# Optimization experiments

Measured on AMD Instinct MI355X. Metric: run time of the kernel, lower is better.

The kernel has to match this reference:

```python
import jax, jax.numpy as jnp
import numpy as np

B, T, I, H = 64, 512, 1024, 1024


def setup_inputs() -> dict:
    key = jax.random.key(0)
    ks = jax.random.split(key, 6)
    s_ih = 1.0 / np.sqrt(I)
    s_hh = 1.0 / np.sqrt(H)
    x = jax.random.normal(ks[0], (B, T, I), dtype=jnp.float32)
    w_ih = jax.random.uniform(ks[1], (4 * H, I), minval=-s_ih, maxval=s_ih, dtype=jnp.float32)
    b_ih = jax.random.uniform(ks[2], (4 * H,), minval=-s_ih, maxval=s_ih, dtype=jnp.float32)
    w_hh = jax.random.uniform(ks[3], (4 * H, H), minval=-s_hh, maxval=s_hh, dtype=jnp.float32)
    b_hh = jax.random.uniform(ks[4], (4 * H,), minval=-s_hh, maxval=s_hh, dtype=jnp.float32)
    # forget_bias = logit(u), u ~ Uniform(1/H, 1-1/H), as in init_hidden
    u = jax.random.uniform(ks[5], (H,), minval=1.0 / H, maxval=1.0 - 1.0 / H, dtype=jnp.float32)
    forget_bias = jnp.log(u / (1.0 - u))
    h0 = jnp.zeros((B, H), dtype=jnp.float32)
    c0 = jnp.zeros((B, H), dtype=jnp.float32)
    return {"x": x, "w_ih": w_ih, "b_ih": b_ih, "w_hh": w_hh, "b_hh": b_hh,
            "forget_bias": forget_bias, "h0": h0, "c0": c0}


def reference(x, w_ih, b_ih, w_hh, b_hh, forget_bias, h0, c0):
    Hd = forget_bias.shape[0]
    # Precompute input projection for all timesteps: [T, B, 4H]
    xW = jnp.einsum('bti,gi->tbg', x, w_ih) + b_ih

    def step(carry, xw_t):
        h, c = carry
        lin = xw_t + h @ w_hh.T + b_hh  # [B, 4H]
        r, f, u, o = jnp.split(lin, 4, axis=1)
        r = jax.nn.sigmoid(r - forget_bias)
        f = jax.nn.sigmoid(f + forget_bias)
        u = jnp.tanh(u)
        o = jax.nn.sigmoid(o)
        g = r * (1.0 - (1.0 - f) ** 2) + (1.0 - r) * f ** 2  # UR gate
        c = g * c + (1.0 - g) * u
        h = o * jnp.tanh(c)
        return (h, c), h

    (h_t, c_t), out = jax.lax.scan(step, (h0, c0), xW)
    out = jnp.swapaxes(out, 0, 1)  # [B, T, H]
    return out, h_t[None], c_t[None]  # h/c with num_layers=1 leading dim
```

## Files before the change

kernel.cpp:

```cpp
#include <hip/hip_runtime.h>
#include <stdint.h>
#include <stddef.h>

typedef __attribute__((ext_vector_type(8))) short short8;
typedef __attribute__((ext_vector_type(4))) float f32x4;
typedef __attribute__((ext_vector_type(2))) float f32x2;

#define MFMA16(A, B, C) __builtin_amdgcn_mfma_f32_16x16x32_bf16((A), (B), (C), 0, 0, 0)

static const size_t OFF_WIH  = 67108864;
static const size_t OFF_WHH  = 75497472;
static const size_t OFF_BIAS = 83886080;
static const size_t OFF_H0   = 83902464;
static const size_t OFF_H1   = 84033536;
static const size_t OFF_FLG  = 84164608;
static const size_t OFF_XW   = 84426752;
static const size_t XW_F32_BYTES = 536870912;

__device__ __forceinline__ unsigned short f2bf(float f) {
    union { float f; uint32_t u; } v; v.f = f;
    uint32_t u = v.u;
    u += 0x7FFFu + ((u >> 16) & 1u);
    return (unsigned short)(u >> 16);
}
__device__ __forceinline__ float bf2f(unsigned short b) {
    union { uint32_t u; float f; } v; v.u = ((uint32_t)b) << 16;
    return v.f;
}

__device__ __forceinline__ float fast_sigmoid(float x) {
    return 1.f / (1.f + __expf(-x));
}
__device__ __forceinline__ float fast_tanh(float x) {
    return 1.f - 2.f / (__expf(2.f * x) + 1.f);
}

__global__ __launch_bounds__(256) void cast4_kernel(const float* __restrict__ s,
                                                    unsigned short* __restrict__ d, int n4) {
    int i = blockIdx.x * 256 + threadIdx.x;
    if (i >= n4) return;
    float4 f = ((const float4*)s)[i];
    ushort4 o;
    o.x = f2bf(f.x); o.y = f2bf(f.y); o.z = f2bf(f.z); o.w = f2bf(f.w);
    ((ushort4*)d)[i] = o;
}

__global__ __launch_bounds__(256) void init_misc(const float* __restrict__ b_ih,
                                                 const float* __restrict__ b_hh,
                                                 float* __restrict__ bias,
                                                 const float* __restrict__ h0,
                                                 unsigned short* __restrict__ h_ini,
                                                 unsigned int* __restrict__ flags) {
    int i = blockIdx.x * 256 + threadIdx.x;
    if (i < 512) flags[i] = 0u;
    if (i < 4096) bias[i] = b_ih[i] + b_hh[i];
    if (i < 65536) h_ini[i] = f2bf(h0[i]);
}

template <bool XWF32>
__global__ __launch_bounds__(512, 2) void fused_kernel(
        unsigned short* hb0, unsigned short* hb1,
        void* xw,
        const unsigned short* __restrict__ whh,
        const unsigned short* __restrict__ wih,
        const float* __restrict__ x,
        const float* __restrict__ bias,
        const float* __restrict__ fb,
        const float* __restrict__ c0,
        float* __restrict__ out,
        float* __restrict__ hcout,
        unsigned int* flags) {
    __shared__ __align__(16) char smem[131072];
    const int tid = threadIdx.x;
    const int wave = tid >> 6, lane = tid & 63;
    unsigned int* xwprog = flags + 256;

    if (blockIdx.x >= 64) {
        unsigned short* As = (unsigned short*)smem;
        unsigned short* Bs = (unsigned short*)(smem + 8192);
        const int g = blockIdx.x - 64;
        const int wm = (wave & 3) * 32, wn = (wave >> 2) * 64;
        const int lr = lane & 15, lk = (lane >> 4) * 8;
        const int r0 = tid >> 2, k0c = (tid & 3) * 8;
        const int rbase = (lane >> 4) * 4;

        for (int tau = g; tau < 8192; tau += 192) {
            const int bm = tau >> 5, bn = tau & 31;
            const int m = bm * 128 + r0;
            const float* pax = x + (size_t)((m & 63) * 512 + (m >> 6)) * 1024 + k0c;
            const unsigned short* pbw = wih + (size_t)(bn * 128 + r0) * 1024 + k0c;
            unsigned short* sa = As + r0 * 32 + k0c;
            unsigned short* sb = Bs + r0 * 32 + k0c;

            f32x4 acc[2][4] = {};
            for (int kk = 0; kk < 32; ++kk) {
                const int ko = kk * 32;
                float4 a0 = *(const float4*)(pax + ko);
                float4 a1 = *(const float4*)(pax + ko + 4);
                uint4 bv = *(const uint4*)(pbw + ko);
                __syncthreads();
                ushort4 ca, cb;
                ca.x = f2bf(a0.x); ca.y = f2bf(a0.y); ca.z = f2bf(a0.z); ca.w = f2bf(a0.w);
                cb.x = f2bf(a1.x); cb.y = f2bf(a1.y); cb.z = f2bf(a1.z); cb.w = f2bf(a1.w);
                *(ushort4*)sa = ca;
                *(ushort4*)(sa + 4) = cb;
                *(uint4*)sb = bv;
                __syncthreads();
                short8 af0 = *(const short8*)(As + (wm + lr) * 32 + lk);
                short8 af1 = *(const short8*)(As + (wm + 16 + lr) * 32 + lk);
                short8 bf4[4];
#pragma unroll
                for (int ni = 0; ni < 4; ++ni)
                    bf4[ni] = *(const short8*)(Bs + (wn + ni * 16 + lr) * 32 + lk);
#pragma unroll
                for (int ni = 0; ni < 4; ++ni) {
                    acc[0][ni] = MFMA16(af0, bf4[ni], acc[0][ni]);
                    acc[1][ni] = MFMA16(af1, bf4[ni], acc[1][ni]);
                }
            }
#pragma unroll
            for (int ni = 0; ni < 4; ++ni) {
                const int gc = bn * 128 + wn + ni * 16 + lr;
                const float bvs = bias[gc];
#pragma unroll
                for (int mi = 0; mi < 2; ++mi) {
                    const int gr = bm * 128 + wm + mi * 16 + rbase;
#pragma unroll
                    for (int r = 0; r < 4; ++r) {
                        const float v = acc[mi][ni][r] + bvs;
                        if constexpr (XWF32) {
                            float* p = (float*)xw + (size_t)(gr + r) * 4096 + gc;
                            asm volatile("global_store_dword %0, %1, off sc1"
                                         :: "v"(p), "v"(v) : "memory");
                        } else {
                            unsigned short* p = (unsigned short*)xw + (size_t)(gr + r) * 4096 + gc;
                            const unsigned int hv = f2bf(v);
                            asm volatile("global_store_short %0, %1, off sc1"
                                         :: "v"(p), "v"(hv) : "memory");
                        }
                    }
                }
            }
            asm volatile("s_waitcnt vmcnt(0)" ::: "memory");
            __syncthreads();
            if (tid == 0)
                __hip_atomic_fetch_add(&xwprog[bm], 1u, __ATOMIC_RELAXED,
                                       __HIP_MEMORY_SCOPE_AGENT);
        }
        return;
    }

    float* part = (float*)smem;
    const int bk = blockIdx.x, ch0 = bk * 16;
    const int kq = wave;
    const int lr = lane & 15, g = lane >> 4;
    unsigned int* ctr = flags;

    short8 Wf[4][4];
#pragma unroll
    for (int ni = 0; ni < 4; ++ni)
#pragma unroll
        for (int ks = 0; ks < 4; ++ks) {
            const unsigned short* p = whh + (size_t)(ni * 1024 + ch0 + lr) * 1024
                                          + kq * 128 + ks * 32 + g * 8;
            asm volatile("global_load_dwordx4 %0, %1, off"
                         : "=&v"(Wf[ni][ks]) : "v"(p));
        }
    asm volatile("s_waitcnt vmcnt(0)" ::: "memory");
    __builtin_amdgcn_sched_barrier(0);

    const int b  = tid >> 3;
    const int j0 = 2 * (tid & 7);
    const int ch = ch0 + j0;
    const float fb0 = fb[ch], fb1 = fb[ch + 1];
    float c0r = c0[b * 1024 + ch], c1r = c0[b * 1024 + ch + 1];

    int wsl[4];
#pragma unroll
    for (int oi = 0; oi < 4; ++oi)
        wsl[oi] = kq * 4096 + lr * 64 + (((oi * 4 + g) ^ (lr & 7)) * 4);
    int rsl[4];
#pragma unroll
    for (int g4 = 0; g4 < 4; ++g4)
        rsl[g4] = b * 64 + (((g4 * 4 + (j0 >> 2)) ^ (b & 7)) * 4) + (j0 & 3);

    const float* xwf = (const float*)xw + (size_t)b * 4096 + ch;
    const unsigned short* xwb = (const unsigned short*)xw + (size_t)b * 4096 + ch;
    float* orun = out + (size_t)b * 524288 + ch;
    unsigned int* my_sig  = &ctr[(bk >> 3) * 32];
    unsigned int* my_poll = &ctr[kq * 32];

    {
        const unsigned int* pr0 = &xwprog[0];
        while (__hip_atomic_load(pr0, __ATOMIC_RELAXED, __HIP_MEMORY_SCOPE_AGENT) < 32u) {}
    }
    __builtin_amdgcn_sched_barrier(0);
    f32x2 xf[4];
    uint32_t xu[4];
    if constexpr (XWF32) {
        asm volatile(
            "global_load_dwordx2 %0, %4, off sc1\n\t"
            "global_load_dwordx2 %1, %5, off sc1\n\t"
            "global_load_dwordx2 %2, %6, off sc1\n\t"
            "global_load_dwordx2 %3, %7, off sc1"
            : "=&v"(xf[0]), "=&v"(xf[1]), "=&v"(xf[2]), "=&v"(xf[3])
            : "v"(xwf), "v"(xwf + 1024), "v"(xwf + 2048), "v"(xwf + 3072));
    } else {
        asm volatile(
            "global_load_dword %0, %4, off sc1\n\t"
            "global_load_dword %1, %5, off sc1\n\t"
            "global_load_dword %2, %6, off sc1\n\t"
            "global_load_dword %3, %7, off sc1"
            : "=&v"(xu[0]), "=&v"(xu[1]), "=&v"(xu[2]), "=&v"(xu[3])
            : "v"(xwb), "v"(xwb + 1024), "v"(xwb + 2048), "v"(xwb + 3072));
    }
    asm volatile("s_waitcnt vmcnt(0)" ::: "memory");
    __builtin_amdgcn_sched_barrier(0);

    float h0v = 0.f, h1v = 0.f;

    for (int t = 0; t < 512; ++t) {
        const unsigned short* hp = (t & 1) ? hb1 : hb0;
        unsigned short* hn       = (t & 1) ? hb0 : hb1;

        if (t > 0) {
            const unsigned tgt = (unsigned)t * 8u;
            while (__hip_atomic_load(my_poll, __ATOMIC_RELAXED,
                                     __HIP_MEMORY_SCOPE_AGENT) < tgt) {}
        }
        __builtin_amdgcn_sched_barrier(0);

        short8 af[4][4];
        {
            const unsigned short* hbase = hp + (size_t)lr * 1024 + kq * 128 + g * 8;
#pragma unroll
            for (int bi = 0; bi < 4; ++bi) {
                const unsigned short* p = hbase + (size_t)bi * 16 * 1024;
                asm volatile(
                    "global_load_dwordx4 %0, %4, off sc1\n\t"
                    "global_load_dwordx4 %1, %4, off offset:64 sc1\n\t"
                    "global_load_dwordx4 %2, %4, off offset:128 sc1\n\t"
                    "global_load_dwordx4 %3, %4, off offset:192 sc1"
                    : "=&v"(af[bi][0]), "=&v"(af[bi][1]),
                      "=&v"(af[bi][2]), "=&v"(af[bi][3])
                    : "v"(p));
            }
        }
        asm volatile("s_waitcnt vmcnt(0)" ::: "memory");
        __builtin_amdgcn_sched_barrier(0);

        f32x4 acc[4][4] = {};
#pragma unroll
        for (int ks = 0; ks < 4; ++ks)
#pragma unroll
            for (int oi = 0; oi < 4; ++oi)
#pragma unroll
                for (int bi = 0; bi < 4; ++bi)
                    acc[oi][bi] = MFMA16(Wf[oi][ks], af[bi][ks], acc[oi][bi]);

#pragma unroll
        for (int oi = 0; oi < 4; ++oi)
#pragma unroll
            for (int bi = 0; bi < 4; ++bi)
                *(f32x4*)&part[wsl[oi] + bi * 1024] = acc[oi][bi];
        __syncthreads();

        float l0[4], l1[4];
#pragma unroll
        for (int g4 = 0; g4 < 4; ++g4) {
            float s0, s1;
            if constexpr (XWF32) { s0 = xf[g4].x; s1 = xf[g4].y; }
            else { s0 = bf2f((unsigned short)xu[g4]);
                   s1 = bf2f((unsigned short)(xu[g4] >> 16)); }
#pragma unroll
            for (int k8 = 0; k8 < 8; ++k8) {
                const float2 v = *(const float2*)&part[k8 * 4096 + rsl[g4]];
                s0 += v.x; s1 += v.y;
            }
            l0[g4] = s0; l1[g4] = s1;
        }
        const float rg0 = fast_sigmoid(l0[0] - fb0);
        const float fg0 = fast_sigmoid(l0[1] + fb0);
        const float ug0 = fast_tanh(l0[2]);
        const float og0 = fast_sigmoid(l0[3]);
        const float rg1 = fast_sigmoid(l1[0] - fb1);
        const float fg1 = fast_sigmoid(l1[1] + fb1);
        const float ug1 = fast_tanh(l1[2]);
        const float og1 = fast_sigmoid(l1[3]);
        const float of0 = 1.f - fg0, of1 = 1.f - fg1;
        const float gg0 = rg0 * (1.f - of0 * of0) + (1.f - rg0) * (fg0 * fg0);
        const float gg1 = rg1 * (1.f - of1 * of1) + (1.f - rg1) * (fg1 * fg1);
        c0r = gg0 * c0r + (1.f - gg0) * ug0;
        c1r = gg1 * c1r + (1.f - gg1) * ug1;
        h0v = og0 * fast_tanh(c0r);
        h1v = og1 * fast_tanh(c1r);

        const unsigned hw = ((unsigned)f2bf(h1v) << 16) | (unsigned)f2bf(h0v);
        __hip_atomic_store((unsigned int*)&hn[b * 1024 + ch], hw,
                           __ATOMIC_RELAXED, __HIP_MEMORY_SCOPE_AGENT);

        __syncthreads();
        if (tid == 0)
            __hip_atomic_fetch_add(my_sig, 1u, __ATOMIC_RELAXED,
                                   __HIP_MEMORY_SCOPE_AGENT);
        __builtin_amdgcn_sched_barrier(0);

        *(f32x2*)orun = (f32x2){h0v, h1v};
        orun += 1024;
        {
            const int tp = (t < 511) ? t + 1 : 511;
            if (!(tp & 1)) {
                const unsigned int* pr = &xwprog[tp >> 1];
                while (__hip_atomic_load(pr, __ATOMIC_RELAXED,
                                         __HIP_MEMORY_SCOPE_AGENT) < 32u) {}
            }
            if constexpr (XWF32) {
                const float* p0 = xwf + (size_t)tp * 262144;
                asm volatile(
                    "global_load_dwordx2 %0, %4, off sc1\n\t"
                    "global_load_dwordx2 %1, %5, off sc1\n\t"
                    "global_load_dwordx2 %2, %6, off sc1\n\t"
                    "global_load_dwordx2 %3, %7, off sc1"
                    : "=&v"(xf[0]), "=&v"(xf[1]), "=&v"(xf[2]), "=&v"(xf[3])
                    : "v"(p0), "v"(p0 + 1024), "v"(p0 + 2048), "v"(p0 + 3072));
            } else {
                const unsigned short* p0 = xwb + (size_t)tp * 262144;
                asm volatile(
                    "global_load_dword %0, %4, off sc1\n\t"
                    "global_load_dword %1, %5, off sc1\n\t"
                    "global_load_dword %2, %6, off sc1\n\t"
                    "global_load_dword %3, %7, off sc1"
                    : "=&v"(xu[0]), "=&v"(xu[1]), "=&v"(xu[2]), "=&v"(xu[3])
                    : "v"(p0), "v"(p0 + 1024), "v"(p0 + 2048), "v"(p0 + 3072));
            }
        }
        asm volatile("s_waitcnt vmcnt(0)" ::: "memory");
        __builtin_amdgcn_sched_barrier(0);
    }

    *(f32x2*)&hcout[b * 1024 + ch] = (f32x2){h0v, h1v};
    *(f32x2*)&hcout[65536 + b * 1024 + ch] = (f32x2){c0r, c1r};
}

extern "C" void kernel_launch(void* const* d_in, const int* in_sizes, int n_in,
                              void* d_out, int out_size, void* d_ws, size_t ws_size,
                              hipStream_t stream) {
    const float* x   = (const float*)d_in[0];
    const float* wih = (const float*)d_in[1];
    const float* bih = (const float*)d_in[2];
    const float* whh = (const float*)d_in[3];
    const float* bhh = (const float*)d_in[4];
    const float* fb  = (const float*)d_in[5];
    const float* h0  = (const float*)d_in[6];
    const float* c0  = (const float*)d_in[7];

    char* ws = (char*)d_ws;
    float* out = (float*)d_out;
    float* hc  = out + 33554432;

    unsigned short* wihb = (unsigned short*)(ws + OFF_WIH);
    unsigned short* whhb = (unsigned short*)(ws + OFF_WHH);
    float* bias          = (float*)(ws + OFF_BIAS);
    unsigned short* hb0  = (unsigned short*)(ws + OFF_H0);
    unsigned short* hb1  = (unsigned short*)(ws + OFF_H1);
    unsigned int* flags  = (unsigned int*)(ws + OFF_FLG);
    void* xw             = (void*)(ws + OFF_XW);

    const bool f32path = ws_size >= OFF_XW + XW_F32_BYTES;

    cast4_kernel<<<4096, 256, 0, stream>>>(wih, wihb, 1048576);
    cast4_kernel<<<4096, 256, 0, stream>>>(whh, whhb, 1048576);
    init_misc<<<256, 256, 0, stream>>>(bih, bhh, bias, h0, hb0, flags);

    const float* xp = x;
    const float* fbp = fb;
    const float* c0p = c0;
    void* xwp = xw;
    const unsigned short* whhp = whhb;
    const unsigned short* wihp = wihb;
    const float* biasp = bias;
    void* kargs[] = { &hb0, &hb1, &xwp, &whhp, &wihp, &xp, &biasp, &fbp, &c0p,
                      &out, &hc, &flags };
    if (f32path)
        hipLaunchCooperativeKernel((void*)fused_kernel<true>, dim3(256), dim3(512),
                                   kargs, 0, stream);
    else
        hipLaunchCooperativeKernel((void*)fused_kernel<false>, dim3(256), dim3(512),
                                   kargs, 0, stream);
}
```

Baseline: 3.690 ms.

## Repartition recurrent LSTM steps to 128 full-K blocks without cross-wave reduction

The recurrent phase moves from 64 blocks, each splitting K across waves with a shared-memory partial-sum reduction, to 128 blocks that each own 8 channels. Every wave now holds the full K range of W_hh in registers, so the smem reduction and its syncs go away, and smaller shared memory may allow higher occupancy. Wave 0 polls eight group counters in parallel before a block barrier, h loads are double-buffered against the MFMAs, and xW producer polling now sleeps between checks. In exchange there are twice as many recurrent blocks to synchronize each step and fewer blocks left for the input projection. It also relies on the unseen launch code changing the grid to match.

```diff
diff --git a/kernel.cpp b/kernel.cpp
--- a/kernel.cpp
+++ b/kernel.cpp
@@ -4,7 +4,6 @@
 
 typedef __attribute__((ext_vector_type(8))) short short8;
 typedef __attribute__((ext_vector_type(4))) float f32x4;
-typedef __attribute__((ext_vector_type(2))) float f32x2;
 
 #define MFMA16(A, B, C) __builtin_amdgcn_mfma_f32_16x16x32_bf16((A), (B), (C), 0, 0, 0)
 
@@ -70,21 +69,21 @@
         float* __restrict__ out,
         float* __restrict__ hcout,
         unsigned int* flags) {
-    __shared__ __align__(16) char smem[131072];
+    __shared__ __align__(16) char smem[16384];
     const int tid = threadIdx.x;
     const int wave = tid >> 6, lane = tid & 63;
     unsigned int* xwprog = flags + 256;
 
-    if (blockIdx.x >= 64) {
+    if (blockIdx.x >= 128) {
         unsigned short* As = (unsigned short*)smem;
         unsigned short* Bs = (unsigned short*)(smem + 8192);
-        const int g = blockIdx.x - 64;
+        const int g = blockIdx.x - 128;
         const int wm = (wave & 3) * 32, wn = (wave >> 2) * 64;
         const int lr = lane & 15, lk = (lane >> 4) * 8;
         const int r0 = tid >> 2, k0c = (tid & 3) * 8;
         const int rbase = (lane >> 4) * 4;
 
-        for (int tau = g; tau < 8192; tau += 192) {
+        for (int tau = g; tau < 8192; tau += 128) {
             const int bm = tau >> 5, bn = tau & 31;
             const int m = bm * 128 + r0;
             const float* pax = x + (size_t)((m & 63) * 512 + (m >> 6)) * 1024 + k0c;
@@ -150,196 +149,212 @@
         return;
     }
 
-    float* part = (float*)smem;
-    const int bk = blockIdx.x, ch0 = bk * 16;
-    const int kq = wave;
-    const int lr = lane & 15, g = lane >> 4;
-    unsigned int* ctr = flags;
-
-    short8 Wf[4][4];
-#pragma unroll
-    for (int ni = 0; ni < 4; ++ni)
-#pragma unroll
-        for (int ks = 0; ks < 4; ++ks) {
-            const unsigned short* p = whh + (size_t)(ni * 1024 + ch0 + lr) * 1024
-                                          + kq * 128 + ks * 32 + g * 8;
-            asm volatile("global_load_dwordx4 %0, %1, off"
-                         : "=&v"(Wf[ni][ks]) : "v"(p));
-        }
-    asm volatile("s_waitcnt vmcnt(0)" ::: "memory");
-    __builtin_amdgcn_sched_barrier(0);
-
-    const int b  = tid >> 3;
-    const int j0 = 2 * (tid & 7);
-    const int ch = ch0 + j0;
-    const float fb0 = fb[ch], fb1 = fb[ch + 1];
-    float c0r = c0[b * 1024 + ch], c1r = c0[b * 1024 + ch + 1];
-
-    int wsl[4];
-#pragma unroll
-    for (int oi = 0; oi < 4; ++oi)
-        wsl[oi] = kq * 4096 + lr * 64 + (((oi * 4 + g) ^ (lr & 7)) * 4);
-    int rsl[4];
-#pragma unroll
-    for (int g4 = 0; g4 < 4; ++g4)
-        rsl[g4] = b * 64 + (((g4 * 4 + (j0 >> 2)) ^ (b & 7)) * 4) + (j0 & 3);
-
-    const float* xwf = (const float*)xw + (size_t)b * 4096 + ch;
-    const unsigned short* xwb = (const unsigned short*)xw + (size_t)b * 4096 + ch;
-    float* orun = out + (size_t)b * 524288 + ch;
-    unsigned int* my_sig  = &ctr[(bk >> 3) * 32];
-    unsigned int* my_poll = &ctr[kq * 32];
-
+    const int rb = blockIdx.x, ch0 = rb * 8;
+    const int ot = wave >> 2, bt = wave & 3;
+    const int lr = lane & 15, g8 = lane >> 4;
+    const int ch = ch0 + ot * 4 + g8;
+    const int batch = bt * 16 + lr;
+    unsigned int* my_sig = &flags[(rb >> 4) * 32];
+
+    short8 Wf[32];
     {
-        const unsigned int* pr0 = &xwprog[0];
-        while (__hip_atomic_load(pr0, __ATOMIC_RELAXED, __HIP_MEMORY_SCOPE_AGENT) < 32u) {}
-    }
-    __builtin_amdgcn_sched_barrier(0);
-    f32x2 xf[4];
-    uint32_t xu[4];
-    if constexpr (XWF32) {
-        asm volatile(
-            "global_load_dwordx2 %0, %4, off sc1\n\t"
-            "global_load_dwordx2 %1, %5, off sc1\n\t"
-            "global_load_dwordx2 %2, %6, off sc1\n\t"
-            "global_load_dwordx2 %3, %7, off sc1"
-            : "=&v"(xf[0]), "=&v"(xf[1]), "=&v"(xf[2]), "=&v"(xf[3])
-            : "v"(xwf), "v"(xwf + 1024), "v"(xwf + 2048), "v"(xwf + 3072));
-    } else {
-        asm volatile(
-            "global_load_dword %0, %4, off sc1\n\t"
-            "global_load_dword %1, %5, off sc1\n\t"
-            "global_load_dword %2, %6, off sc1\n\t"
-            "global_load_dword %3, %7, off sc1"
-            : "=&v"(xu[0]), "=&v"(xu[1]), "=&v"(xu[2]), "=&v"(xu[3])
-            : "v"(xwb), "v"(xwb + 1024), "v"(xwb + 2048), "v"(xwb + 3072));
+        const unsigned short* wp = whh + (size_t)((lr & 3) * 1024 + ch0 + ot * 4 + (lr >> 2)) * 1024
+                                        + g8 * 8;
+#pragma unroll
+        for (int cc = 0; cc < 8; ++cc) {
+            const unsigned short* p = wp + cc * 128;
+            asm volatile(
+                "global_load_dwordx4 %0, %4, off\n\t"
+                "global_load_dwordx4 %1, %4, off offset:64\n\t"
+                "global_load_dwordx4 %2, %4, off offset:128\n\t"
+                "global_load_dwordx4 %3, %4, off offset:192"
+                : "=&v"(Wf[cc * 4]), "=&v"(Wf[cc * 4 + 1]),
+                  "=&v"(Wf[cc * 4 + 2]), "=&v"(Wf[cc * 4 + 3])
+                : "v"(p));
+        }
     }
     asm volatile("s_waitcnt vmcnt(0)" ::: "memory");
     __builtin_amdgcn_sched_barrier(0);
 
-    float h0v = 0.f, h1v = 0.f;
+    const float fbv = fb[ch];
+    float cr = c0[batch * 1024 + ch];
+    const float* xwf = (const float*)xw + (size_t)batch * 4096 + ch;
+    const unsigned short* xwb = (const unsigned short*)xw + (size_t)batch * 4096 + ch;
+    float* orun = out + (size_t)batch * 524288 + ch;
+
+    while (__hip_atomic_load(&xwprog[0], __ATOMIC_RELAXED, __HIP_MEMORY_SCOPE_AGENT) < 32u)
+        __builtin_amdgcn_s_sleep(2);
+    __builtin_amdgcn_sched_barrier(0);
+    float xwv[4];
+    {
+        uint32_t r0_, r1_, r2_, r3_;
+        if constexpr (XWF32) {
+            asm volatile(
+                "global_load_dword %0, %4, off sc1\n\t"
+                "global_load_dword %1, %5, off sc1\n\t"
+                "global_load_dword %2, %6, off sc1\n\t"
+                "global_load_dword %3, %7, off sc1\n\t"
+                "s_waitcnt vmcnt(0)"
+                : "=&v"(r0_), "=&v"(r1_), "=&v"(r2_), "=&v"(r3_)
+                : "v"(xwf), "v"(xwf + 1024), "v"(xwf + 2048), "v"(xwf + 3072));
+            union { uint32_t u; float f; } u0{r0_}, u1{r1_}, u2{r2_}, u3{r3_};
+            xwv[0] = u0.f; xwv[1] = u1.f; xwv[2] = u2.f; xwv[3] = u3.f;
+        } else {
+            asm volatile(
+                "global_load_ushort %0, %4, off sc1\n\t"
+                "global_load_ushort %1, %5, off sc1\n\t"
+                "global_load_ushort %2, %6, off sc1\n\t"
+                "global_load_ushort %3, %7, off sc1\n\t"
+                "s_waitcnt vmcnt(0)"
+                : "=&v"(r0_), "=&v"(r1_), "=&v"(r2_), "=&v"(r3_)
+                : "v"(xwb), "v"(xwb + 1024), "v"(xwb + 2048), "v"(xwb + 3072));
+            xwv[0] = bf2f((unsigned short)r0_); xwv[1] = bf2f((unsigned short)r1_);
+            xwv[2] = bf2f((unsigned short)r2_); xwv[3] = bf2f((unsigned short)r3_);
+        }
+    }
+    __builtin_amdgcn_sched_barrier(0);
+
+    float hv = 0.f;
 
     for (int t = 0; t < 512; ++t) {
         const unsigned short* hp = (t & 1) ? hb1 : hb0;
         unsigned short* hn       = (t & 1) ? hb0 : hb1;
 
         if (t > 0) {
-            const unsigned tgt = (unsigned)t * 8u;
-            while (__hip_atomic_load(my_poll, __ATOMIC_RELAXED,
-                                     __HIP_MEMORY_SCOPE_AGENT) < tgt) {}
-        }
-        __builtin_amdgcn_sched_barrier(0);
-
-        short8 af[4][4];
-        {
-            const unsigned short* hbase = hp + (size_t)lr * 1024 + kq * 128 + g * 8;
-#pragma unroll
-            for (int bi = 0; bi < 4; ++bi) {
-                const unsigned short* p = hbase + (size_t)bi * 16 * 1024;
-                asm volatile(
-                    "global_load_dwordx4 %0, %4, off sc1\n\t"
-                    "global_load_dwordx4 %1, %4, off offset:64 sc1\n\t"
-                    "global_load_dwordx4 %2, %4, off offset:128 sc1\n\t"
-                    "global_load_dwordx4 %3, %4, off offset:192 sc1"
-                    : "=&v"(af[bi][0]), "=&v"(af[bi][1]),
-                      "=&v"(af[bi][2]), "=&v"(af[bi][3])
-                    : "v"(p));
-            }
-        }
+            if (wave == 0) {
+                const unsigned tgt = 16u * (unsigned)t;
+                for (;;) {
+                    uint32_t c0_, c1_, c2_, c3_, c4_, c5_, c6_, c7_;
+                    asm volatile(
+                        "global_load_dword %0, %8, off sc1\n\t"
+                        "global_load_dword %1, %8, off offset:128 sc1\n\t"
+                        "global_load_dword %2, %8, off offset:256 sc1\n\t"
+                        "global_load_dword %3, %8, off offset:384 sc1\n\t"
+                        "global_load_dword %4, %8, off offset:512 sc1\n\t"
+                        "global_load_dword %5, %8, off offset:640 sc1\n\t"
+                        "global_load_dword %6, %8, off offset:768 sc1\n\t"
+                        "global_load_dword %7, %8, off offset:896 sc1\n\t"
+                        "s_waitcnt vmcnt(0)"
+                        : "=&v"(c0_), "=&v"(c1_), "=&v"(c2_), "=&v"(c3_),
+                          "=&v"(c4_), "=&v"(c5_), "=&v"(c6_), "=&v"(c7_)
+                        : "v"(flags));
+                    uint32_t m0 = c0_ < c1_ ? c0_ : c1_;
+                    uint32_t m1 = c2_ < c3_ ? c2_ : c3_;
+                    uint32_t m2 = c4_ < c5_ ? c4_ : c5_;
+                    uint32_t m3 = c6_ < c7_ ? c6_ : c7_;
+                    m0 = m0 < m1 ? m0 : m1;
+                    m2 = m2 < m3 ? m2 : m3;
+                    if ((m0 < m2 ? m0 : m2) >= tgt) break;
+                }
+            }
+            __builtin_amdgcn_sched_barrier(0);
+            __builtin_amdgcn_s_barrier();
+        }
+
+        const unsigned short* hb = hp + (size_t)batch * 1024 + g8 * 8;
+        short8 af0[8], af1[8];
+#define LOAD_CHUNK(BUF, CC)                                                     \
+        {                                                                       \
+            const unsigned short* p = hb + (CC) * 256;                          \
+            asm volatile(                                                       \
+                "global_load_dwordx4 %0, %8, off sc1\n\t"                       \
+                "global_load_dwordx4 %1, %8, off offset:64 sc1\n\t"             \
+                "global_load_dwordx4 %2, %8, off offset:128 sc1\n\t"            \
+                "global_load_dwordx4 %3, %8, off offset:192 sc1\n\t"            \
+                "global_load_dwordx4 %4, %8, off offset:256 sc1\n\t"            \
+                "global_load_dwordx4 %5, %8, off offset:320 sc1\n\t"            \
+                "global_load_dwordx4 %6, %8, off offset:384 sc1\n\t"            \
+                "global_load_dwordx4 %7, %8, off offset:448 sc1"                \
+                : "=&v"(BUF[0]), "=&v"(BUF[1]), "=&v"(BUF[2]), "=&v"(BUF[3]),   \
+                  "=&v"(BUF[4]), "=&v"(BUF[5]), "=&v"(BUF[6]), "=&v"(BUF[7])    \
+                : "v"(p));                                                      \
+        }
+        LOAD_CHUNK(af0, 0)
+        f32x4 acc0 = {}, acc1 = {};
+#pragma unroll
+        for (int cc = 0; cc < 4; ++cc) {
+            if (cc == 0) { LOAD_CHUNK(af1, 1) }
+            else if (cc == 1) { LOAD_CHUNK(af0, 2) }
+            else if (cc == 2) { LOAD_CHUNK(af1, 3) }
+            if (cc < 3) asm volatile("s_waitcnt vmcnt(8)" ::: "memory");
+            else        asm volatile("s_waitcnt vmcnt(0)" ::: "memory");
+            __builtin_amdgcn_sched_barrier(0);
+#pragma unroll
+            for (int j = 0; j < 8; ++j) {
+                const short8 a = (cc & 1) ? af1[j] : af0[j];
+                if (j & 1) acc1 = MFMA16(Wf[cc * 8 + j], a, acc1);
+                else       acc0 = MFMA16(Wf[cc * 8 + j], a, acc0);
+            }
+        }
+#undef LOAD_CHUNK
+
+        const float lr_ = acc0[0] + acc1[0] + xwv[0];
+        const float lf  = acc0[1] + acc1[1] + xwv[1];
+        const float lu  = acc0[2] + acc1[2] + xwv[2];
+        const float lo  = acc0[3] + acc1[3] + xwv[3];
+        const float rg = fast_sigmoid(lr_ - fbv);
+        const float fg = fast_sigmoid(lf + fbv);
+        const float ug = fast_tanh(lu);
+        const float og = fast_sigmoid(lo);
+        const float of = 1.f - fg;
+        const float gg = rg * (1.f - of * of) + (1.f - rg) * (fg * fg);
+        cr = gg * cr + (1.f - gg) * ug;
+        hv = og * fast_tanh(cr);
+
+        const unsigned hw = (unsigned)f2bf(hv);
+        asm volatile("global_store_short %0, %1, off sc1"
+                     :: "v"(hn + batch * 1024 + ch), "v"(hw) : "memory");
         asm volatile("s_waitcnt vmcnt(0)" ::: "memory");
         __builtin_amdgcn_sched_barrier(0);
-
-        f32x4 acc[4][4] = {};
-#pragma unroll
-        for (int ks = 0; ks < 4; ++ks)
-#pragma unroll
-            for (int oi = 0; oi < 4; ++oi)
-#pragma unroll
-                for (int bi = 0; bi < 4; ++bi)
-                    acc[oi][bi] = MFMA16(Wf[oi][ks], af[bi][ks], acc[oi][bi]);
-
-#pragma unroll
-        for (int oi = 0; oi < 4; ++oi)
-#pragma unroll
-            for (int bi = 0; bi < 4; ++bi)
-                *(f32x4*)&part[wsl[oi] + bi * 1024] = acc[oi][bi];
-        __syncthreads();
-
-        float l0[4], l1[4];
-#pragma unroll
-        for (int g4 = 0; g4 < 4; ++g4) {
-            float s0, s1;
-            if constexpr (XWF32) { s0 = xf[g4].x; s1 = xf[g4].y; }
-            else { s0 = bf2f((unsigned short)xu[g4]);
-                   s1 = bf2f((unsigned short)(xu[g4] >> 16)); }
-#pragma unroll
-            for (int k8 = 0; k8 < 8; ++k8) {
-                const float2 v = *(const float2*)&part[k8 * 4096 + rsl[g4]];
-                s0 += v.x; s1 += v.y;
-            }
-            l0[g4] = s0; l1[g4] = s1;
-        }
-        const float rg0 = fast_sigmoid(l0[0] - fb0);
-        const float fg0 = fast_sigmoid(l0[1] + fb0);
-        const float ug0 = fast_tanh(l0[2]);
-        const float og0 = fast_sigmoid(l0[3]);
-        const float rg1 = fast_sigmoid(l1[0] - fb1);
-        const float fg1 = fast_sigmoid(l1[1] + fb1);
-        const float ug1 = fast_tanh(l1[2]);
-        const float og1 = fast_sigmoid(l1[3]);
-        const float of0 = 1.f - fg0, of1 = 1.f - fg1;
-        const float gg0 = rg0 * (1.f - of0 * of0) + (1.f - rg0) * (fg0 * fg0);
-        const float gg1 = rg1 * (1.f - of1 * of1) + (1.f - rg1) * (fg1 * fg1);
-        c0r = gg0 * c0r + (1.f - gg0) * ug0;
-        c1r = gg1 * c1r + (1.f - gg1) * ug1;
-        h0v = og0 * fast_tanh(c0r);
-        h1v = og1 * fast_tanh(c1r);
-
-        const unsigned hw = ((unsigned)f2bf(h1v) << 16) | (unsigned)f2bf(h0v);
-        __hip_atomic_store((unsigned int*)&hn[b * 1024 + ch], hw,
-                           __ATOMIC_RELAXED, __HIP_MEMORY_SCOPE_AGENT);
-
-        __syncthreads();
+        __builtin_amdgcn_s_barrier();
         if (tid == 0)
             __hip_atomic_fetch_add(my_sig, 1u, __ATOMIC_RELAXED,
                                    __HIP_MEMORY_SCOPE_AGENT);
         __builtin_amdgcn_sched_barrier(0);
 
-        *(f32x2*)orun = (f32x2){h0v, h1v};
+        *orun = hv;
         orun += 1024;
+        if (t == 511) {
+            hcout[batch * 1024 + ch] = hv;
+            hcout[65536 + batch * 1024 + ch] = cr;
+        }
         {
             const int tp = (t < 511) ? t + 1 : 511;
             if (!(tp & 1)) {
-                const unsigned int* pr = &xwprog[tp >> 1];
-                while (__hip_atomic_load(pr, __ATOMIC_RELAXED,
-                                         __HIP_MEMORY_SCOPE_AGENT) < 32u) {}
-            }
+                while (__hip_atomic_load(&xwprog[tp >> 1], __ATOMIC_RELAXED,
+                                         __HIP_MEMORY_SCOPE_AGENT) < 32u)
+                    __builtin_amdgcn_s_sleep(2);
+            }
+            uint32_t r0_, r1_, r2_, r3_;
             if constexpr (XWF32) {
                 const float* p0 = xwf + (size_t)tp * 262144;
-                asm volatile(
-                    "global_load_dwordx2 %0, %4, off sc1\n\t"
-                    "global_load_dwordx2 %1, %5, off sc1\n\t"
-                    "global_load_dwordx2 %2, %6, off sc1\n\t"
-                    "global_load_dwordx2 %3, %7, off sc1"
-                    : "=&v"(xf[0]), "=&v"(xf[1]), "=&v"(xf[2]), "=&v"(xf[3])
-                    : "v"(p0), "v"(p0 + 1024), "v"(p0 + 2048), "v"(p0 + 3072));
-            } else {
-                const unsigned short* p0 = xwb + (size_t)tp * 262144;
                 asm volatile(
                     "global_load_dword %0, %4, off sc1\n\t"
                     "global_load_dword %1, %5, off sc1\n\t"
                     "global_load_dword %2, %6, off sc1\n\t"
-                    "global_load_dword %3, %7, off sc1"
-                    : "=&v"(xu[0]), "=&v"(xu[1]), "=&v"(xu[2]), "=&v"(xu[3])
+                    "global_load_dword %3, %7, off sc1\n\t"
+                    "s_waitcnt vmcnt(0)"
+                    : "=&v"(r0_), "=&v"(r1_), "=&v"(r2_), "=&v"(r3_)
                     : "v"(p0), "v"(p0 + 1024), "v"(p0 + 2048), "v"(p0 + 3072));
+                union { uint32_t u; float f; } u0{r0_}, u1{r1_}, u2{r2_}, u3{r3_};
+                xwv[0] = u0.f; xwv[1] = u1.f; xwv[2] = u2.f; xwv[3] = u3.f;
+            } else {
+                const unsigned short* p0 = xwb + (size_t)tp * 262144;
+                asm volatile(
+                    "global_load_ushort %0, %4, off sc1\n\t"
+                    "global_load_ushort %1, %5, off sc1\n\t"
+                    "global_load_ushort %2, %6, off sc1\n\t"
+                    "global_load_ushort %3, %7, off sc1\n\t"
+                    "s_waitcnt vmcnt(0)"
+                    : "=&v"(r0_), "=&v"(r1_), "=&v"(r2_), "=&v"(r3_)
+                    : "v"(p0), "v"(p0 + 1024), "v"(p0 + 2048), "v"(p0 + 3072));
+                xwv[0] = bf2f((unsigned short)r0_); xwv[1] = bf2f((unsigned short)r1_);
+                xwv[2] = bf2f((unsigned short)r2_); xwv[3] = bf2f((unsigned short)r3_);
             }
         }
         asm volatile("s_waitcnt vmcnt(0)" ::: "memory");
         __builtin_amdgcn_sched_barrier(0);
     }
-
-    *(f32x2*)&hcout[b * 1024 + ch] = (f32x2){h0v, h1v};
-    *(f32x2*)&hcout[65536 + b * 1024 + ch] = (f32x2){c0r, c1r};
 }
 
 extern "C" void kernel_launch(void* const* d_in, const int* in_sizes, int n_in,
```

Result: slower. 5.112 ms (+38.5%).
